# Performance work log

Hardware: AMD Instinct MI355X
Metric: run time of the kernel (lower is better)

The kernel has to match this reference:

```python
import jax, jax.numpy as jnp
import numpy as np

B, S, D, H = 2, 4096, 512, 8
DH = D // H  # head dim = 64


def setup_inputs() -> dict:
    key = jax.random.key(0)
    ks = jax.random.split(key, 5)
    s = 1.0 / np.sqrt(D)
    return {
        "x": jax.random.normal(ks[0], (B, S, D), jnp.float32),
        "Wq": jax.random.normal(ks[1], (D, D), jnp.float32) * s,
        "bq": jnp.zeros((D,), jnp.float32),
        "Wk": jax.random.normal(ks[2], (D, D), jnp.float32) * s,
        "bk": jnp.zeros((D,), jnp.float32),
        "Wv": jax.random.normal(ks[3], (D, D), jnp.float32) * s,
        "bv": jnp.zeros((D,), jnp.float32),
        "Wo": jax.random.normal(ks[4], (D, D), jnp.float32) * s,
        "bo": jnp.zeros((D,), jnp.float32),
    }


def _split_heads(t):  # [B,S,D] -> [B,H,S,DH]
    return t.reshape(B, S, H, DH).transpose(0, 2, 1, 3)


def reference(x, Wq, bq, Wk, bk, Wv, bv, Wo, bo):
    relu = jax.nn.relu
    # linear projections with activation (keras MultiHeadAttention applies
    # the activation to all Q/K/V/output mappings)
    q = _split_heads(relu(x @ Wq + bq))
    k = _split_heads(relu(x @ Wk + bk))
    v = _split_heads(relu(x @ Wv + bv))
    # scaled dot-product attention; scale uses per-head feature dim (DH)
    e = jnp.einsum("bhqd,bhkd->bhqk", q, k) / jnp.sqrt(jnp.float32(DH))
    attn = jax.nn.softmax(e, axis=-1)  # stable max-subtract softmax
    o = jnp.einsum("bhqk,bhkd->bhqd", attn, v)
    o = o.transpose(0, 2, 1, 3).reshape(B, S, D)  # merge heads
    return relu(o @ Wo + bo)
```

## Files before the change

kernel.cpp:

```cpp
#include <hip/hip_runtime.h>
#include <stdint.h>

#define B_ 2
#define S_ 4096
#define D_ 512
#define H_ 8
#define DH_ 64
#define M_ (B_*S_)
#define LOG2E 1.4426950408889634f

typedef unsigned short u16;
typedef __bf16 bf16x8 __attribute__((ext_vector_type(8)));
typedef __bf16 bf16x4 __attribute__((ext_vector_type(4)));
typedef float f32x4 __attribute__((ext_vector_type(4)));

#if defined(__has_builtin)
#if __has_builtin(__builtin_amdgcn_exp2f)
#define EXP2(x) __builtin_amdgcn_exp2f(x)
#else
#define EXP2(x) exp2f(x)
#endif
#else
#define EXP2(x) exp2f(x)
#endif

__device__ __forceinline__ u16 f2bf(float f) {
  __bf16 b = (__bf16)f;
  return __builtin_bit_cast(u16, b);
}

__device__ __forceinline__ void gl_lds16(const void* g, void* l) {
  __builtin_amdgcn_global_load_lds(
      (__attribute__((address_space(1))) void*)(void*)g,
      (__attribute__((address_space(3))) void*)l, 16, 0, 0);
}

#define MM(a, b, c) __builtin_amdgcn_mfma_f32_16x16x32_bf16((a), (b), (c), 0, 0, 0)
#define LD8(p) (*(const bf16x8*)(p))

__global__ void k_cvt(const float* __restrict__ x, u16* __restrict__ xb, int n4) {
  int i = blockIdx.x * 256 + threadIdx.x;
  if (i < n4) {
    float4 v = ((const float4*)x)[i];
    bf16x4 o;
    o[0] = (__bf16)v.x; o[1] = (__bf16)v.y; o[2] = (__bf16)v.z; o[3] = (__bf16)v.w;
    ((bf16x4*)xb)[i] = o;
  }
}

__global__ void k_twt(const float* __restrict__ w0, const float* __restrict__ w1,
                      const float* __restrict__ w2, const float* __restrict__ w3,
                      u16* __restrict__ t0, u16* __restrict__ t1,
                      u16* __restrict__ t2, u16* __restrict__ t3) {
  __shared__ float t[32][33];
  int z = blockIdx.z;
  const float* w = z == 0 ? w0 : z == 1 ? w1 : z == 2 ? w2 : w3;
  u16* wt       = z == 0 ? t0 : z == 1 ? t1 : z == 2 ? t2 : t3;
  int n0 = blockIdx.x * 32, k0 = blockIdx.y * 32;
  int tx = threadIdx.x, ty = threadIdx.y;
  #pragma unroll
  for (int j = 0; j < 4; j++) t[ty + 8*j][tx] = w[(k0 + ty + 8*j) * D_ + n0 + tx];
  __syncthreads();
  #pragma unroll
  for (int j = 0; j < 4; j++) wt[(n0 + ty + 8*j) * D_ + k0 + tx] = f2bf(t[tx][ty + 8*j]);
}

__device__ __forceinline__
void gemm_body(const u16* __restrict__ A, const u16* __restrict__ Bt,
               const float* __restrict__ bias, void* __restrict__ out,
               float scale, int mode) {
  __shared__ __align__(16) u16 Al[128*64];
  __shared__ __align__(16) u16 Bl[128*64];
  int tid = threadIdx.x;
  int lane = tid & 63, w = tid >> 6;
  int wr = w >> 2, wc = w & 3;
  int g = lane >> 4, qi = lane & 15;
  int m0 = blockIdx.y * 128, n0 = blockIdx.x * 128;
  int swzc = ((lane & 7) ^ (lane >> 3)) * 8;
  int lr8 = lane >> 3;

  f32x4 acc[4][2] = {};

  for (int k0 = 0; k0 < D_; k0 += 64) {
    #pragma unroll
    for (int j = 0; j < 2; j++) {
      int r0 = (w*2 + j) * 8;
      gl_lds16(A  + (m0 + r0 + lr8) * D_ + k0 + swzc, &Al[r0 * 64]);
      gl_lds16(Bt + (n0 + r0 + lr8) * D_ + k0 + swzc, &Bl[r0 * 64]);
    }
    __syncthreads();
    #pragma unroll
    for (int h = 0; h < 2; h++) {
      bf16x8 a[4], bq[2];
      #pragma unroll
      for (int i = 0; i < 4; i++) {
        int row = wr*64 + i*16 + qi;
        int c = (h*4 + g) ^ (row & 7);
        a[i] = LD8(&Al[row*64 + c*8]);
      }
      #pragma unroll
      for (int jn = 0; jn < 2; jn++) {
        int row = wc*32 + jn*16 + qi;
        int c = (h*4 + g) ^ (row & 7);
        bq[jn] = LD8(&Bl[row*64 + c*8]);
      }
      #pragma unroll
      for (int i = 0; i < 4; i++)
        #pragma unroll
        for (int jn = 0; jn < 2; jn++)
          acc[i][jn] = MM(a[i], bq[jn], acc[i][jn]);
    }
    __syncthreads();
  }

  #pragma unroll
  for (int i = 0; i < 4; i++)
    #pragma unroll
    for (int jn = 0; jn < 2; jn++) {
      int col = n0 + wc*32 + jn*16 + qi;
      float bs = bias[col];
      if (mode == 1) {
        int row0 = m0 + wr*64 + i*16 + g*4;
        int bb = row0 >> 12, ss0 = row0 & (S_ - 1);
        int hh = col >> 6, dd = col & 63;
        bf16x4 pk;
        pk[0] = (__bf16)(fmaxf(acc[i][jn][0] + bs, 0.0f) * scale);
        pk[1] = (__bf16)(fmaxf(acc[i][jn][1] + bs, 0.0f) * scale);
        pk[2] = (__bf16)(fmaxf(acc[i][jn][2] + bs, 0.0f) * scale);
        pk[3] = (__bf16)(fmaxf(acc[i][jn][3] + bs, 0.0f) * scale);
        *(bf16x4*)&((u16*)out)[((bb*H_ + hh)*DH_ + dd)*S_ + ss0] = pk;
      } else {
        #pragma unroll
        for (int ii = 0; ii < 4; ii++) {
          int row = m0 + wr*64 + i*16 + g*4 + ii;
          float v = fmaxf(acc[i][jn][ii] + bs, 0.0f) * scale;
          if (mode == 2) {
            ((float*)out)[row * D_ + col] = v;
          } else {
            int bb = row >> 12, ss = row & (S_ - 1);
            int hh = col >> 6, dd = col & 63;
            ((u16*)out)[((bb*H_ + hh)*S_ + ss)*DH_ + dd] = f2bf(v);
          }
        }
      }
    }
}

__global__ __launch_bounds__(512, 2)
void k_qkv(const u16* __restrict__ A,
           const u16* __restrict__ btq, const u16* __restrict__ btk, const u16* __restrict__ btv,
           const float* __restrict__ bq, const float* __restrict__ bk, const float* __restrict__ bv,
           u16* __restrict__ q, u16* __restrict__ k, u16* __restrict__ v) {
  int z = blockIdx.z;
  if (z == 0)      gemm_body(A, btq, bq, q, 0.125f * LOG2E, 0);
  else if (z == 1) gemm_body(A, btk, bk, k, 1.0f, 0);
  else             gemm_body(A, btv, bv, v, 1.0f, 1);
}

__global__ __launch_bounds__(512, 2)
void k_go(const u16* __restrict__ A, const u16* __restrict__ bt,
          const float* __restrict__ bias, float* __restrict__ out) {
  gemm_body(A, bt, bias, out, 1.0f, 2);
}

__global__ __launch_bounds__(256, 4)
void k_attn(const u16* __restrict__ Q, const u16* __restrict__ K,
            const u16* __restrict__ Vt, u16* __restrict__ O) {
  __shared__ __align__(16) u16 Kl[2][64*64];
  __shared__ __align__(16) u16 Vl[2][64*64];
  __shared__ __align__(16) u16 Pl[4][16*64];
  const int tid = threadIdx.x;
  const int lane = tid & 63, w = tid >> 6;
  const int g = lane >> 4, qi = lane & 15, qi7 = qi & 7;

  const int bid = blockIdx.x;
  const int xcd = bid & 7, idx = bid >> 3;
  const int hb = xcd * 2 + (idx & 1);
  const int qt = idx >> 1;
  const int b = hb >> 3, h = hb & 7;

  const u16* Qh = Q  + ((b*H_ + h) * S_) * DH_;
  const u16* Kh = K  + ((b*H_ + h) * S_) * DH_;
  const u16* Vh = Vt + ((b*H_ + h) * DH_) * S_;
  const int q0 = qt*64 + w*16;

  const bf16x8 aq0 = LD8(&Qh[(q0 + qi)*DH_ + g*8]);
  const bf16x8 aq1 = LD8(&Qh[(q0 + qi)*DH_ + 32 + g*8]);

  f32x4 oacc0 = {}, oacc1 = {}, oacc2 = {}, oacc3 = {};
  const f32x4 zro = {0.f, 0.f, 0.f, 0.f};
  float lrow = 0.0f;

  const int swzc = ((lane & 7) ^ (lane >> 3)) * 8;
  const int lr8 = lane >> 3;

  int fo[4][2];
  #pragma unroll
  for (int rt = 0; rt < 4; rt++)
    #pragma unroll
    for (int kh = 0; kh < 2; kh++)
      fo[rt][kh] = (rt*16 + qi)*128 + (((kh*4 + g) ^ qi7)*16);
  int pw[4];
  #pragma unroll
  for (int kt = 0; kt < 4; kt++)
    pw[kt] = qi*128 + (((kt*2 + (g >> 1)) ^ qi7)*16) + (g & 1)*8;
  const int pr0 = qi*128 + ((g ^ qi7)*16);
  const int pr1 = qi*128 + (((4 + g) ^ qi7)*16);
  char* Pw = (char*)Pl[w];

  const u16* kp0 = Kh + (w*16 + lr8)*DH_ + swzc;
  const u16* kp1 = kp0 + 8*DH_;
  const u16* vp0 = Vh + (w*16 + lr8)*S_ + swzc;
  const u16* vp1 = vp0 + 8*S_;
  u16* kdst[2][2];
  u16* vdst[2][2];
  #pragma unroll
  for (int bb2 = 0; bb2 < 2; bb2++)
    #pragma unroll
    for (int j = 0; j < 2; j++) {
      kdst[bb2][j] = &Kl[bb2][(w*16 + j*8)*64];
      vdst[bb2][j] = &Vl[bb2][(w*16 + j*8)*64];
    }

  gl_lds16(kp0, kdst[0][0]);
  gl_lds16(kp1, kdst[0][1]);
  gl_lds16(vp0, vdst[0][0]);
  gl_lds16(vp1, vdst[0][1]);
  kp0 += 64*DH_; kp1 += 64*DH_; vp0 += 64; vp1 += 64;

#define TILE(BUF, LAST) { \
  if (!(LAST)) { \
    gl_lds16(kp0, kdst[(BUF)^1][0]); \
    gl_lds16(kp1, kdst[(BUF)^1][1]); \
    gl_lds16(vp0, vdst[(BUF)^1][0]); \
    gl_lds16(vp1, vdst[(BUF)^1][1]); \
    kp0 += 64*DH_; kp1 += 64*DH_; vp0 += 64; vp1 += 64; \
    asm volatile("s_waitcnt vmcnt(4)" ::: "memory"); \
  } else { \
    asm volatile("s_waitcnt vmcnt(0)" ::: "memory"); \
  } \
  __builtin_amdgcn_s_barrier(); \
  __builtin_amdgcn_sched_barrier(0); \
  const char* Kb = (const char*)Kl[(BUF)]; \
  const char* Vb = (const char*)Vl[(BUF)]; \
  f32x4 s0, s1, s2, s3; \
  { f32x4 z = MM(LD8(Kb + fo[0][0]), aq0, zro); s0 = MM(LD8(Kb + fo[0][1]), aq1, z); } \
  { f32x4 z = MM(LD8(Kb + fo[1][0]), aq0, zro); s1 = MM(LD8(Kb + fo[1][1]), aq1, z); } \
  { f32x4 z = MM(LD8(Kb + fo[2][0]), aq0, zro); s2 = MM(LD8(Kb + fo[2][1]), aq1, z); } \
  { f32x4 z = MM(LD8(Kb + fo[3][0]), aq0, zro); s3 = MM(LD8(Kb + fo[3][1]), aq1, z); } \
  float e0  = EXP2(s0[0]), e1  = EXP2(s0[1]), e2  = EXP2(s0[2]), e3  = EXP2(s0[3]); \
  float e4  = EXP2(s1[0]), e5  = EXP2(s1[1]), e6  = EXP2(s1[2]), e7  = EXP2(s1[3]); \
  float e8  = EXP2(s2[0]), e9  = EXP2(s2[1]), e10 = EXP2(s2[2]), e11 = EXP2(s2[3]); \
  float e12 = EXP2(s3[0]), e13 = EXP2(s3[1]), e14 = EXP2(s3[2]), e15 = EXP2(s3[3]); \
  { bf16x4 p; p[0]=(__bf16)e0;  p[1]=(__bf16)e1;  p[2]=(__bf16)e2;  p[3]=(__bf16)e3;  *(bf16x4*)(Pw + pw[0]) = p; } \
  { bf16x4 p; p[0]=(__bf16)e4;  p[1]=(__bf16)e5;  p[2]=(__bf16)e6;  p[3]=(__bf16)e7;  *(bf16x4*)(Pw + pw[1]) = p; } \
  { bf16x4 p; p[0]=(__bf16)e8;  p[1]=(__bf16)e9;  p[2]=(__bf16)e10; p[3]=(__bf16)e11; *(bf16x4*)(Pw + pw[2]) = p; } \
  { bf16x4 p; p[0]=(__bf16)e12; p[1]=(__bf16)e13; p[2]=(__bf16)e14; p[3]=(__bf16)e15; *(bf16x4*)(Pw + pw[3]) = p; } \
  lrow += (((e0+e1)+(e2+e3)) + ((e4+e5)+(e6+e7))) + (((e8+e9)+(e10+e11)) + ((e12+e13)+(e14+e15))); \
  __builtin_amdgcn_s_setprio(1); \
  { bf16x8 ap = LD8(Pw + pr0); \
    oacc0 = MM(ap, LD8(Vb + fo[0][0]), oacc0); \
    oacc1 = MM(ap, LD8(Vb + fo[1][0]), oacc1); \
    oacc2 = MM(ap, LD8(Vb + fo[2][0]), oacc2); \
    oacc3 = MM(ap, LD8(Vb + fo[3][0]), oacc3); } \
  { bf16x8 ap = LD8(Pw + pr1); \
    oacc0 = MM(ap, LD8(Vb + fo[0][1]), oacc0); \
    oacc1 = MM(ap, LD8(Vb + fo[1][1]), oacc1); \
    oacc2 = MM(ap, LD8(Vb + fo[2][1]), oacc2); \
    oacc3 = MM(ap, LD8(Vb + fo[3][1]), oacc3); } \
  __builtin_amdgcn_s_setprio(0); \
  __builtin_amdgcn_sched_barrier(0); \
  __builtin_amdgcn_s_barrier(); \
}

  for (int i = 0; i < 31; ++i) {
    TILE(0, 0)
    TILE(1, 0)
  }
  TILE(0, 0)
  TILE(1, 1)
#undef TILE

  lrow += __shfl_xor(lrow, 16);
  lrow += __shfl_xor(lrow, 32);
  float rv = 1.0f / lrow;
  float rr[4];
  #pragma unroll
  for (int i = 0; i < 4; i++) rr[i] = __shfl(rv, g*4 + i);
  #pragma unroll
  for (int ii = 0; ii < 4; ii++) {
    int row = q0 + g*4 + ii;
    u16* orow = O + (b*S_ + row)*D_ + h*64 + qi;
    orow[0]  = f2bf(oacc0[ii] * rr[ii]);
    orow[16] = f2bf(oacc1[ii] * rr[ii]);
    orow[32] = f2bf(oacc2[ii] * rr[ii]);
    orow[48] = f2bf(oacc3[ii] * rr[ii]);
  }
}

extern "C" void kernel_launch(void* const* d_in, const int* in_sizes, int n_in,
                              void* d_out, int out_size, void* d_ws, size_t ws_size,
                              hipStream_t stream) {
  (void)in_sizes; (void)n_in; (void)out_size; (void)ws_size;
  const float* x  = (const float*)d_in[0];
  const float* Wq = (const float*)d_in[1];
  const float* bq = (const float*)d_in[2];
  const float* Wk = (const float*)d_in[3];
  const float* bk = (const float*)d_in[4];
  const float* Wv = (const float*)d_in[5];
  const float* bv = (const float*)d_in[6];
  const float* Wo = (const float*)d_in[7];
  const float* bo = (const float*)d_in[8];

  char* ws = (char*)d_ws;
  u16* xb  = (u16*)ws;
  u16* wtq = (u16*)(ws + 8388608);
  u16* wtk = wtq + 512*512;
  u16* wtv = wtk + 512*512;
  u16* wto = wtv + 512*512;
  u16* Qh  = (u16*)(ws + 8388608 + 4*524288);
  u16* Kh  = Qh + M_*D_;
  u16* Vt  = Kh + M_*D_;
  u16* Ob  = xb;

  k_cvt<<<4096, 256, 0, stream>>>(x, xb, M_*D_/4);
  k_twt<<<dim3(16,16,4), dim3(32,8), 0, stream>>>(Wq, Wk, Wv, Wo, wtq, wtk, wtv, wto);
  k_qkv<<<dim3(4,64,3), 512, 0, stream>>>(xb, wtq, wtk, wtv, bq, bk, bv, Qh, Kh, Vt);
  k_attn<<<1024, 256, 0, stream>>>(Qh, Kh, Vt, Ob);
  k_go<<<dim3(4,64), 512, 0, stream>>>(Ob, wto, bo, (float*)d_out);
}
```

Before: 215.2 us.

## Process two 16-row query tiles per wave in attention to reuse K/V loads

Each wave now handles 32 query rows (two 16-row MFMA tiles) instead of 16, so each K and V fragment read from LDS feeds two MFMAs. The block covers 128 queries, the grid is halved to 512 blocks, and the P scratch buffer doubles. This halves K/V global-to-LDS traffic and LDS fragment reads per query. The cost is more registers (launch bounds lowered to 2 blocks per SM) and fewer blocks, which may hurt occupancy and latency hiding.

```diff
diff --git a/kernel.cpp b/kernel.cpp
--- a/kernel.cpp
+++ b/kernel.cpp
@@ -163,12 +163,78 @@
   gemm_body(A, bt, bias, out, 1.0f, 2);
 }
 
-__global__ __launch_bounds__(256, 4)
+template<int BUF, int LAST>
+__device__ __forceinline__ void attn_tile(
+    const u16*& kp0, const u16*& kp1, const u16*& vp0, const u16*& vp1,
+    u16* (&kdst)[2][2], u16* (&vdst)[2][2],
+    const u16* Kl0, const u16* Kl1, const u16* Vl0, const u16* Vl1,
+    char* Pw, const int (&fo)[4][2], const int (&pwo)[4], int pr0, int pr1,
+    bf16x8 aqA0, bf16x8 aqA1, bf16x8 aqB0, bf16x8 aqB1,
+    f32x4 (&oA)[4], f32x4 (&oB)[4], float& lA, float& lB) {
+  if (!LAST) {
+    gl_lds16(kp0, kdst[BUF^1][0]);
+    gl_lds16(kp1, kdst[BUF^1][1]);
+    gl_lds16(vp0, vdst[BUF^1][0]);
+    gl_lds16(vp1, vdst[BUF^1][1]);
+    kp0 += 64*DH_; kp1 += 64*DH_; vp0 += 64; vp1 += 64;
+    asm volatile("s_waitcnt vmcnt(4)" ::: "memory");
+  } else {
+    asm volatile("s_waitcnt vmcnt(0)" ::: "memory");
+  }
+  __builtin_amdgcn_s_barrier();
+  __builtin_amdgcn_sched_barrier(0);
+  const char* Kb = (const char*)(BUF ? Kl1 : Kl0);
+  const char* Vb = (const char*)(BUF ? Vl1 : Vl0);
+  const f32x4 zro = {0.f, 0.f, 0.f, 0.f};
+
+  f32x4 sA[4], sB[4];
+  #pragma unroll
+  for (int kt = 0; kt < 4; kt++) {
+    bf16x8 k0 = LD8(Kb + fo[kt][0]);
+    bf16x8 k1 = LD8(Kb + fo[kt][1]);
+    sA[kt] = MM(k1, aqA1, MM(k0, aqA0, zro));
+    sB[kt] = MM(k1, aqB1, MM(k0, aqB0, zro));
+  }
+
+  float suA = 0.0f, suB = 0.0f;
+  #pragma unroll
+  for (int kt = 0; kt < 4; kt++) {
+    float a0 = EXP2(sA[kt][0]), a1 = EXP2(sA[kt][1]);
+    float a2 = EXP2(sA[kt][2]), a3 = EXP2(sA[kt][3]);
+    suA += (a0+a1)+(a2+a3);
+    bf16x4 pa; pa[0]=(__bf16)a0; pa[1]=(__bf16)a1; pa[2]=(__bf16)a2; pa[3]=(__bf16)a3;
+    *(bf16x4*)(Pw + pwo[kt]) = pa;
+    float b0 = EXP2(sB[kt][0]), b1 = EXP2(sB[kt][1]);
+    float b2 = EXP2(sB[kt][2]), b3 = EXP2(sB[kt][3]);
+    suB += (b0+b1)+(b2+b3);
+    bf16x4 pb; pb[0]=(__bf16)b0; pb[1]=(__bf16)b1; pb[2]=(__bf16)b2; pb[3]=(__bf16)b3;
+    *(bf16x4*)(Pw + 2048 + pwo[kt]) = pb;
+  }
+  lA += suA; lB += suB;
+
+  __builtin_amdgcn_s_setprio(1);
+  #pragma unroll
+  for (int kh = 0; kh < 2; kh++) {
+    bf16x8 apA = LD8(Pw + (kh ? pr1 : pr0));
+    bf16x8 apB = LD8(Pw + 2048 + (kh ? pr1 : pr0));
+    #pragma unroll
+    for (int nt = 0; nt < 4; nt++) {
+      bf16x8 vf = LD8(Vb + fo[nt][kh]);
+      oA[nt] = MM(apA, vf, oA[nt]);
+      oB[nt] = MM(apB, vf, oB[nt]);
+    }
+  }
+  __builtin_amdgcn_s_setprio(0);
+  __builtin_amdgcn_sched_barrier(0);
+  __builtin_amdgcn_s_barrier();
+}
+
+__global__ __launch_bounds__(256, 2)
 void k_attn(const u16* __restrict__ Q, const u16* __restrict__ K,
             const u16* __restrict__ Vt, u16* __restrict__ O) {
   __shared__ __align__(16) u16 Kl[2][64*64];
   __shared__ __align__(16) u16 Vl[2][64*64];
-  __shared__ __align__(16) u16 Pl[4][16*64];
+  __shared__ __align__(16) u16 Pl[4][32*64];
   const int tid = threadIdx.x;
   const int lane = tid & 63, w = tid >> 6;
   const int g = lane >> 4, qi = lane & 15, qi7 = qi & 7;
@@ -182,14 +248,15 @@
   const u16* Qh = Q  + ((b*H_ + h) * S_) * DH_;
   const u16* Kh = K  + ((b*H_ + h) * S_) * DH_;
   const u16* Vh = Vt + ((b*H_ + h) * DH_) * S_;
-  const int q0 = qt*64 + w*16;
-
-  const bf16x8 aq0 = LD8(&Qh[(q0 + qi)*DH_ + g*8]);
-  const bf16x8 aq1 = LD8(&Qh[(q0 + qi)*DH_ + 32 + g*8]);
-
-  f32x4 oacc0 = {}, oacc1 = {}, oacc2 = {}, oacc3 = {};
-  const f32x4 zro = {0.f, 0.f, 0.f, 0.f};
-  float lrow = 0.0f;
+  const int q0 = qt*128 + w*32;
+
+  const bf16x8 aqA0 = LD8(&Qh[(q0 + qi)*DH_ + g*8]);
+  const bf16x8 aqA1 = LD8(&Qh[(q0 + qi)*DH_ + 32 + g*8]);
+  const bf16x8 aqB0 = LD8(&Qh[(q0 + 16 + qi)*DH_ + g*8]);
+  const bf16x8 aqB1 = LD8(&Qh[(q0 + 16 + qi)*DH_ + 32 + g*8]);
+
+  f32x4 oA[4] = {}, oB[4] = {};
+  float lA = 0.0f, lB = 0.0f;
 
   const int swzc = ((lane & 7) ^ (lane >> 3)) * 8;
   const int lr8 = lane >> 3;
@@ -200,10 +267,10 @@
     #pragma unroll
     for (int kh = 0; kh < 2; kh++)
       fo[rt][kh] = (rt*16 + qi)*128 + (((kh*4 + g) ^ qi7)*16);
-  int pw[4];
+  int pwo[4];
   #pragma unroll
   for (int kt = 0; kt < 4; kt++)
-    pw[kt] = qi*128 + (((kt*2 + (g >> 1)) ^ qi7)*16) + (g & 1)*8;
+    pwo[kt] = qi*128 + (((kt*2 + (g >> 1)) ^ qi7)*16) + (g & 1)*8;
   const int pr0 = qi*128 + ((g ^ qi7)*16);
   const int pr1 = qi*128 + (((4 + g) ^ qi7)*16);
   char* Pw = (char*)Pl[w];
@@ -228,73 +295,40 @@
   gl_lds16(vp1, vdst[0][1]);
   kp0 += 64*DH_; kp1 += 64*DH_; vp0 += 64; vp1 += 64;
 
-#define TILE(BUF, LAST) { \
-  if (!(LAST)) { \
-    gl_lds16(kp0, kdst[(BUF)^1][0]); \
-    gl_lds16(kp1, kdst[(BUF)^1][1]); \
-    gl_lds16(vp0, vdst[(BUF)^1][0]); \
-    gl_lds16(vp1, vdst[(BUF)^1][1]); \
-    kp0 += 64*DH_; kp1 += 64*DH_; vp0 += 64; vp1 += 64; \
-    asm volatile("s_waitcnt vmcnt(4)" ::: "memory"); \
-  } else { \
-    asm volatile("s_waitcnt vmcnt(0)" ::: "memory"); \
-  } \
-  __builtin_amdgcn_s_barrier(); \
-  __builtin_amdgcn_sched_barrier(0); \
-  const char* Kb = (const char*)Kl[(BUF)]; \
-  const char* Vb = (const char*)Vl[(BUF)]; \
-  f32x4 s0, s1, s2, s3; \
-  { f32x4 z = MM(LD8(Kb + fo[0][0]), aq0, zro); s0 = MM(LD8(Kb + fo[0][1]), aq1, z); } \
-  { f32x4 z = MM(LD8(Kb + fo[1][0]), aq0, zro); s1 = MM(LD8(Kb + fo[1][1]), aq1, z); } \
-  { f32x4 z = MM(LD8(Kb + fo[2][0]), aq0, zro); s2 = MM(LD8(Kb + fo[2][1]), aq1, z); } \
-  { f32x4 z = MM(LD8(Kb + fo[3][0]), aq0, zro); s3 = MM(LD8(Kb + fo[3][1]), aq1, z); } \
-  float e0  = EXP2(s0[0]), e1  = EXP2(s0[1]), e2  = EXP2(s0[2]), e3  = EXP2(s0[3]); \
-  float e4  = EXP2(s1[0]), e5  = EXP2(s1[1]), e6  = EXP2(s1[2]), e7  = EXP2(s1[3]); \
-  float e8  = EXP2(s2[0]), e9  = EXP2(s2[1]), e10 = EXP2(s2[2]), e11 = EXP2(s2[3]); \
-  float e12 = EXP2(s3[0]), e13 = EXP2(s3[1]), e14 = EXP2(s3[2]), e15 = EXP2(s3[3]); \
-  { bf16x4 p; p[0]=(__bf16)e0;  p[1]=(__bf16)e1;  p[2]=(__bf16)e2;  p[3]=(__bf16)e3;  *(bf16x4*)(Pw + pw[0]) = p; } \
-  { bf16x4 p; p[0]=(__bf16)e4;  p[1]=(__bf16)e5;  p[2]=(__bf16)e6;  p[3]=(__bf16)e7;  *(bf16x4*)(Pw + pw[1]) = p; } \
-  { bf16x4 p; p[0]=(__bf16)e8;  p[1]=(__bf16)e9;  p[2]=(__bf16)e10; p[3]=(__bf16)e11; *(bf16x4*)(Pw + pw[2]) = p; } \
-  { bf16x4 p; p[0]=(__bf16)e12; p[1]=(__bf16)e13; p[2]=(__bf16)e14; p[3]=(__bf16)e15; *(bf16x4*)(Pw + pw[3]) = p; } \
-  lrow += (((e0+e1)+(e2+e3)) + ((e4+e5)+(e6+e7))) + (((e8+e9)+(e10+e11)) + ((e12+e13)+(e14+e15))); \
-  __builtin_amdgcn_s_setprio(1); \
-  { bf16x8 ap = LD8(Pw + pr0); \
-    oacc0 = MM(ap, LD8(Vb + fo[0][0]), oacc0); \
-    oacc1 = MM(ap, LD8(Vb + fo[1][0]), oacc1); \
-    oacc2 = MM(ap, LD8(Vb + fo[2][0]), oacc2); \
-    oacc3 = MM(ap, LD8(Vb + fo[3][0]), oacc3); } \
-  { bf16x8 ap = LD8(Pw + pr1); \
-    oacc0 = MM(ap, LD8(Vb + fo[0][1]), oacc0); \
-    oacc1 = MM(ap, LD8(Vb + fo[1][1]), oacc1); \
-    oacc2 = MM(ap, LD8(Vb + fo[2][1]), oacc2); \
-    oacc3 = MM(ap, LD8(Vb + fo[3][1]), oacc3); } \
-  __builtin_amdgcn_s_setprio(0); \
-  __builtin_amdgcn_sched_barrier(0); \
-  __builtin_amdgcn_s_barrier(); \
-}
+#define T(BUF, LAST) attn_tile<BUF, LAST>(kp0, kp1, vp0, vp1, kdst, vdst, \
+    &Kl[0][0], &Kl[1][0], &Vl[0][0], &Vl[1][0], Pw, fo, pwo, pr0, pr1, \
+    aqA0, aqA1, aqB0, aqB1, oA, oB, lA, lB)
 
   for (int i = 0; i < 31; ++i) {
-    TILE(0, 0)
-    TILE(1, 0)
-  }
-  TILE(0, 0)
-  TILE(1, 1)
-#undef TILE
-
-  lrow += __shfl_xor(lrow, 16);
-  lrow += __shfl_xor(lrow, 32);
-  float rv = 1.0f / lrow;
-  float rr[4];
-  #pragma unroll
-  for (int i = 0; i < 4; i++) rr[i] = __shfl(rv, g*4 + i);
+    T(0, 0);
+    T(1, 0);
+  }
+  T(0, 0);
+  T(1, 1);
+#undef T
+
+  lA += __shfl_xor(lA, 16); lA += __shfl_xor(lA, 32);
+  lB += __shfl_xor(lB, 16); lB += __shfl_xor(lB, 32);
+  float rvA = 1.0f / lA, rvB = 1.0f / lB;
+  float rrA[4], rrB[4];
+  #pragma unroll
+  for (int i = 0; i < 4; i++) {
+    rrA[i] = __shfl(rvA, g*4 + i);
+    rrB[i] = __shfl(rvB, g*4 + i);
+  }
   #pragma unroll
   for (int ii = 0; ii < 4; ii++) {
-    int row = q0 + g*4 + ii;
-    u16* orow = O + (b*S_ + row)*D_ + h*64 + qi;
-    orow[0]  = f2bf(oacc0[ii] * rr[ii]);
-    orow[16] = f2bf(oacc1[ii] * rr[ii]);
-    orow[32] = f2bf(oacc2[ii] * rr[ii]);
-    orow[48] = f2bf(oacc3[ii] * rr[ii]);
+    int rowA = q0 + g*4 + ii;
+    u16* oaro = O + (b*S_ + rowA)*D_ + h*64 + qi;
+    oaro[0]  = f2bf(oA[0][ii] * rrA[ii]);
+    oaro[16] = f2bf(oA[1][ii] * rrA[ii]);
+    oaro[32] = f2bf(oA[2][ii] * rrA[ii]);
+    oaro[48] = f2bf(oA[3][ii] * rrA[ii]);
+    u16* obro = oaro + 16*D_;
+    obro[0]  = f2bf(oB[0][ii] * rrB[ii]);
+    obro[16] = f2bf(oB[1][ii] * rrB[ii]);
+    obro[32] = f2bf(oB[2][ii] * rrB[ii]);
+    obro[48] = f2bf(oB[3][ii] * rrB[ii]);
   }
 }
 
@@ -326,6 +360,6 @@
   k_cvt<<<4096, 256, 0, stream>>>(x, xb, M_*D_/4);
   k_twt<<<dim3(16,16,4), dim3(32,8), 0, stream>>>(Wq, Wk, Wv, Wo, wtq, wtk, wtv, wto);
   k_qkv<<<dim3(4,64,3), 512, 0, stream>>>(xb, wtq, wtk, wtv, bq, bk, bv, Qh, Kh, Vt);
-  k_attn<<<1024, 256, 0, stream>>>(Qh, Kh, Vt, Ob);
+  k_attn<<<512, 256, 0, stream>>>(Qh, Kh, Vt, Ob);
   k_go<<<dim3(4,64), 512, 0, stream>>>(Ob, wto, bo, (float*)d_out);
 }
```

Measured after the change: 203.7 us. -5.4%, faster.
